# Kernel optimization log

Measured on AMD Instinct MI355X. Metric: run time of the kernel, lower is better.

The kernel has to match this reference:

```python
import jax, jax.numpy as jnp
import numpy as np

N = 100_000  # nodes
E = 1_200_000  # edges (avg degree 12)
EPS = 1e-5


def setup_inputs() -> dict:
    key = jax.random.key(0)
    ks = jax.random.split(key, 12)

    def w(k, shape):
        fan_in = shape[0]
        return jax.random.normal(k, shape, dtype=jnp.float32) * (1.0 / np.sqrt(fan_in))

    return {
        "x": jax.random.normal(ks[0], (N, 4), dtype=jnp.float32),
        "edge_index": jax.random.randint(ks[1], (2, E), 0, N, dtype=jnp.int32),
        "W1": w(ks[2], (4, 16)), "b1": jnp.zeros(16, jnp.float32),
        "g1": jnp.ones(16, jnp.float32), "bt1": jnp.zeros(16, jnp.float32),
        "W2": w(ks[3], (16, 32)), "b2": jnp.zeros(32, jnp.float32),
        "g2": jnp.ones(32, jnp.float32), "bt2": jnp.zeros(32, jnp.float32),
        "W3": w(ks[4], (32, 64)), "b3": jnp.zeros(64, jnp.float32),
        "g3": jnp.ones(64, jnp.float32), "bt3": jnp.zeros(64, jnp.float32),
        "Wf1": w(ks[5], (64, 32)), "bf1": jnp.zeros(32, jnp.float32),
        "Wf2": w(ks[6], (32, 16)), "bf2": jnp.zeros(16, jnp.float32),
        "Wf3": w(ks[7], (16, 2)), "bf3": jnp.zeros(2, jnp.float32),
    }


def _gcn_conv(x, W, b, src, dst):
    """PyG GCNConv: self-loops + symmetric deg^-1/2 normalization + scatter-add."""
    n = x.shape[0]
    h = x @ W  # [N, out]
    loop = jnp.arange(n, dtype=src.dtype)
    s = jnp.concatenate([src, loop])  # [E+N]
    d = jnp.concatenate([dst, loop])
    deg = jax.ops.segment_sum(jnp.ones_like(d, dtype=h.dtype), d, num_segments=n)
    dinv = jnp.where(deg > 0, jax.lax.rsqrt(deg), 0.0)
    norm = dinv[s] * dinv[d]  # [E+N]
    out = jax.ops.segment_sum(h[s] * norm[:, None], d, num_segments=n)
    return out + b


def _bn(x, g, bt):
    # BatchNorm1d over node dim (batch statistics, training-mode semantics)
    m = jnp.mean(x, axis=0)
    v = jnp.var(x, axis=0)
    return (x - m) * jax.lax.rsqrt(v + EPS) * g + bt


def reference(x, edge_index, W1, b1, g1, bt1, W2, b2, g2, bt2, W3, b3, g3, bt3,
              Wf1, bf1, Wf2, bf2, Wf3, bf3):
    src, dst = edge_index[0], edge_index[1]
    h = jax.nn.elu(_bn(jax.nn.relu(_gcn_conv(x, W1, b1, src, dst)), g1, bt1))
    h = jax.nn.elu(_bn(jax.nn.relu(_gcn_conv(h, W2, b2, src, dst)), g2, bt2))
    h = jax.nn.elu(_bn(jax.nn.relu(_gcn_conv(h, W3, b3, src, dst)), g3, bt3))
    h = jax.nn.elu(h @ Wf1 + bf1)
    h = jax.nn.elu(h @ Wf2 + bf2)
    h = h @ Wf3 + bf3
    return jax.nn.log_softmax(h, axis=1)
```

## Files before the change

kernel.cpp:

```cpp
#include <hip/hip_runtime.h>
#include <hip/hip_fp16.h>
#include <math.h>

#define BN_EPS 1e-5f

__device__ inline float4 f4add(float4 a, float4 b) {
  return make_float4(a.x + b.x, a.y + b.y, a.z + b.z, a.w + b.w);
}

union H8 {
  float4 f4;
  __half2 h2[4];
};


__global__ void hist_kernel(const int* __restrict__ dst, int* __restrict__ bcount, int e) {
  __shared__ int h[512];
  for (int i = threadIdx.x; i < 512; i += 256) h[i] = 0;
  __syncthreads();
  int stride = gridDim.x * 256;
  for (int i = blockIdx.x * 256 + threadIdx.x; i < e; i += stride)
    atomicAdd(&h[dst[i] >> 8], 1);
  __syncthreads();
  for (int i = threadIdx.x; i < 512; i += 256)
    if (h[i] > 0) atomicAdd(&bcount[i], h[i]);
}

__global__ void scan_buckets(const int* __restrict__ bcount, int* __restrict__ boffset,
                             int* __restrict__ bcursor, int* __restrict__ row_start,
                             int nbuck, int n, int e) {
  __shared__ int sc[512];
  int tid = threadIdx.x;
  int v = (tid < nbuck) ? bcount[tid] : 0;
  sc[tid] = v;
  __syncthreads();
  for (int off = 1; off < 512; off <<= 1) {
    int add = (tid >= off) ? sc[tid - off] : 0;
    __syncthreads();
    sc[tid] += add;
    __syncthreads();
  }
  int excl = sc[tid] - v;
  if (tid <= nbuck) {
    int val = (tid < nbuck) ? excl : e;
    boffset[tid] = val;
    bcursor[tid] = val;
  }
  if (tid == 0) row_start[n] = e;
}

__global__ void partition_kernel(const int* __restrict__ src, const int* __restrict__ dst,
                                 int* __restrict__ bcursor, int2* __restrict__ ebuf, int e) {
  __shared__ int h[512];
  __shared__ int base[512];
  const int BLK_E = 4096;
  int e0 = blockIdx.x * BLK_E;
  int e1 = min(e0 + BLK_E, e);
  for (int i = threadIdx.x; i < 512; i += 256) h[i] = 0;
  __syncthreads();
  for (int i = e0 + threadIdx.x; i < e1; i += 256)
    atomicAdd(&h[dst[i] >> 8], 1);
  __syncthreads();
  for (int i = threadIdx.x; i < 512; i += 256) {
    int c = h[i];
    base[i] = (c > 0) ? atomicAdd(&bcursor[i], c) : 0;
    h[i] = 0;
  }
  __syncthreads();
  for (int i = e0 + threadIdx.x; i < e1; i += 256) {
    int d = dst[i];
    int b = d >> 8;
    int r = atomicAdd(&h[b], 1);
    ebuf[base[b] + r] = make_int2(src[i], d);
  }
}

__global__ void bucket_fill(const int2* __restrict__ ebuf, const int* __restrict__ boffset,
                            int* __restrict__ row_start, float* __restrict__ dinv,
                            int* __restrict__ csr_src, int n) {
  __shared__ int lcnt[256];
  __shared__ int lpre[256];
  int bid = blockIdx.x;
  int nb0 = bid << 8;
  int tid = threadIdx.x;
  int e0 = boffset[bid], e1 = boffset[bid + 1];
  lcnt[tid] = 0;
  __syncthreads();
  for (int j = e0 + tid; j < e1; j += 256)
    atomicAdd(&lcnt[ebuf[j].y - nb0], 1);
  __syncthreads();
  int v = lcnt[tid];
  lpre[tid] = v;
  __syncthreads();
  for (int off = 1; off < 256; off <<= 1) {
    int add = (tid >= off) ? lpre[tid - off] : 0;
    __syncthreads();
    lpre[tid] += add;
    __syncthreads();
  }
  int excl = lpre[tid] - v;
  int node = nb0 + tid;
  if (node < n) {
    row_start[node] = e0 + excl;
    dinv[node] = rsqrtf((float)(v + 1));
  }
  __syncthreads();
  lpre[tid] = excl;
  __syncthreads();
  for (int j = e0 + tid; j < e1; j += 256) {
    int2 ed = ebuf[j];
    int p = atomicAdd(&lpre[ed.y - nb0], 1);
    csr_src[e0 + p] = ed.x;
  }
}

template <int K, int C, bool BN>
__global__ __launch_bounds__(256) void mm_dinv_h(
    const float* __restrict__ X, const float* __restrict__ stats,
    const float* __restrict__ g, const float* __restrict__ bt,
    const float* __restrict__ W, const float* __restrict__ dinv,
    float4* __restrict__ hh, int n) {
  constexpr int GP8 = C / 8;
  __shared__ float w[K * C];
  __shared__ float bsc[K], bsh[K];
  for (int i = threadIdx.x; i < K * C; i += 256) w[i] = W[i];
  if (BN && threadIdx.x < K) {
    int c = threadIdx.x;
    float inv_n = 1.0f / (float)n;
    float m = stats[c] * inv_n;
    float var = fmaxf(stats[K + c] * inv_n - m * m, 0.f);
    float sc = rsqrtf(var + BN_EPS) * g[c];
    bsc[c] = sc;
    bsh[c] = bt[c] - m * sc;
  }
  __syncthreads();

  int idx = blockIdx.x * 256 + threadIdx.x;
  if (idx >= n * GP8) return;
  int nn = idx / GP8;
  int c8 = idx % GP8;

  float acc[8];
#pragma unroll
  for (int t = 0; t < 8; t++) acc[t] = 0.f;

  const float4* row4 = (const float4*)(X + (size_t)nn * K);
#pragma unroll
  for (int k4 = 0; k4 < K / 4; k4++) {
    float4 xv = row4[k4];
#pragma unroll
    for (int j = 0; j < 4; j++) {
      int k = k4 * 4 + j;
      float v = (j == 0) ? xv.x : (j == 1) ? xv.y : (j == 2) ? xv.z : xv.w;
      if (BN) {
        v = v * bsc[k] + bsh[k];
        v = v > 0.f ? v : (expf(v) - 1.f);
      }
      int wb = k * C + c8 * 8;
#pragma unroll
      for (int t = 0; t < 8; t++) acc[t] += v * w[wb + t];
    }
  }
  float dn = dinv[nn];
  H8 o;
#pragma unroll
  for (int q = 0; q < 4; q++)
    o.h2[q] = __float22half2_rn(make_float2(acc[2 * q] * dn, acc[2 * q + 1] * dn));
  hh[idx] = o.f4;
}

template <int C, int LOGGP>
__global__ __launch_bounds__(256) void gather_finalize_h(
    const float4* __restrict__ hh8, const int* __restrict__ row_start,
    const int* __restrict__ csr_src, const float* __restrict__ dinv,
    const float* __restrict__ bias, float4* __restrict__ act4, int n) {
  constexpr int GP = C / 8;
  constexpr int GP4 = C / 4;
  constexpr int NPB = 256 / GP;
  int tid = threadIdx.x;
  int c8 = tid & (GP - 1);
  int local = tid >> LOGGP;
  int n0 = blockIdx.x * NPB + local;
  if (n0 >= n) return;

  float acc[8];
  {
    H8 u;
    u.f4 = hh8[n0 * GP + c8];
#pragma unroll
    for (int q = 0; q < 4; q++) {
      float2 f = __half22float2(u.h2[q]);
      acc[2 * q] = f.x;
      acc[2 * q + 1] = f.y;
    }
  }
  int s = row_start[n0], e0 = row_start[n0 + 1];
  int j = s;
  for (; j + 4 <= e0; j += 4) {
    int i0 = csr_src[j];
    int i1 = csr_src[j + 1];
    int i2 = csr_src[j + 2];
    int i3 = csr_src[j + 3];
    H8 u0, u1, u2, u3;
    u0.f4 = hh8[i0 * GP + c8];
    u1.f4 = hh8[i1 * GP + c8];
    u2.f4 = hh8[i2 * GP + c8];
    u3.f4 = hh8[i3 * GP + c8];
#pragma unroll
    for (int q = 0; q < 4; q++) {
      float2 f0 = __half22float2(u0.h2[q]);
      float2 f1 = __half22float2(u1.h2[q]);
      float2 f2 = __half22float2(u2.h2[q]);
      float2 f3 = __half22float2(u3.h2[q]);
      acc[2 * q] += (f0.x + f1.x) + (f2.x + f3.x);
      acc[2 * q + 1] += (f0.y + f1.y) + (f2.y + f3.y);
    }
  }
  for (; j < e0; j++) {
    H8 u;
    u.f4 = hh8[csr_src[j] * GP + c8];
#pragma unroll
    for (int q = 0; q < 4; q++) {
      float2 f = __half22float2(u.h2[q]);
      acc[2 * q] += f.x;
      acc[2 * q + 1] += f.y;
    }
  }

  float dn = dinv[n0];
  const float4* bias4 = (const float4*)bias;
  float4 blo = bias4[c8 * 2], bhi = bias4[c8 * 2 + 1];
  float4 v0, v1;
  v0.x = fmaxf(dn * acc[0] + blo.x, 0.f);
  v0.y = fmaxf(dn * acc[1] + blo.y, 0.f);
  v0.z = fmaxf(dn * acc[2] + blo.z, 0.f);
  v0.w = fmaxf(dn * acc[3] + blo.w, 0.f);
  v1.x = fmaxf(dn * acc[4] + bhi.x, 0.f);
  v1.y = fmaxf(dn * acc[5] + bhi.y, 0.f);
  v1.z = fmaxf(dn * acc[6] + bhi.z, 0.f);
  v1.w = fmaxf(dn * acc[7] + bhi.w, 0.f);
  act4[n0 * GP4 + c8 * 2] = v0;
  act4[n0 * GP4 + c8 * 2 + 1] = v1;
}

template <int C>
__global__ void stats_kernel(const float4* __restrict__ act4, float* __restrict__ stats, int n) {
  constexpr int GP = C / 4;
  constexpr int NPB = 256 / GP;
  int tid = threadIdx.x;
  int c4 = tid & (GP - 1);
  int local = tid / GP;
  float4 s = make_float4(0.f, 0.f, 0.f, 0.f);
  float4 q = make_float4(0.f, 0.f, 0.f, 0.f);
  for (int n0 = blockIdx.x * NPB + local; n0 < n; n0 += gridDim.x * NPB) {
    float4 v = act4[n0 * GP + c4];
    s = f4add(s, v);
    q.x += v.x * v.x; q.y += v.y * v.y; q.z += v.z * v.z; q.w += v.w * v.w;
  }
  __shared__ float4 redS[256];
  __shared__ float4 redQ[256];
  redS[tid] = s;
  redQ[tid] = q;
  __syncthreads();
#pragma unroll
  for (int off = 128; off >= GP; off >>= 1) {
    if (tid < off) {
      redS[tid] = f4add(redS[tid], redS[tid + off]);
      redQ[tid] = f4add(redQ[tid], redQ[tid + off]);
    }
    __syncthreads();
  }
  if (tid < GP) {
    atomicAdd(&stats[4 * tid + 0], redS[tid].x);
    atomicAdd(&stats[4 * tid + 1], redS[tid].y);
    atomicAdd(&stats[4 * tid + 2], redS[tid].z);
    atomicAdd(&stats[4 * tid + 3], redS[tid].w);
    atomicAdd(&stats[C + 4 * tid + 0], redQ[tid].x);
    atomicAdd(&stats[C + 4 * tid + 1], redQ[tid].y);
    atomicAdd(&stats[C + 4 * tid + 2], redQ[tid].z);
    atomicAdd(&stats[C + 4 * tid + 3], redQ[tid].w);
  }
}


__global__ __launch_bounds__(256) void head_kernel(
    const float* __restrict__ h,
    const float* __restrict__ st3, const float* __restrict__ g3,
    const float* __restrict__ bt3,
    const float* __restrict__ Wf1, const float* __restrict__ bf1,
    const float* __restrict__ Wf2, const float* __restrict__ bf2,
    const float* __restrict__ Wf3, const float* __restrict__ bf3,
    float* __restrict__ out, int n) {
  __shared__ float w1[64 * 32], w2[32 * 16], w3[16 * 2];
  __shared__ float sb1[32], sb2[16], sb3[2];
  __shared__ float bsc[64], bsh[64];
  for (int i = threadIdx.x; i < 64 * 32; i += 256) w1[i] = Wf1[i];
  for (int i = threadIdx.x; i < 32 * 16; i += 256) w2[i] = Wf2[i];
  if (threadIdx.x < 64) {
    int c = threadIdx.x;
    float inv_n = 1.0f / (float)n;
    float m = st3[c] * inv_n;
    float var = fmaxf(st3[64 + c] * inv_n - m * m, 0.f);
    float sc = rsqrtf(var + BN_EPS) * g3[c];
    bsc[c] = sc;
    bsh[c] = bt3[c] - m * sc;
  }
  if (threadIdx.x < 32) {
    w3[threadIdx.x] = Wf3[threadIdx.x];
    sb1[threadIdx.x] = bf1[threadIdx.x];
  }
  if (threadIdx.x < 16) sb2[threadIdx.x] = bf2[threadIdx.x];
  if (threadIdx.x < 2) sb3[threadIdx.x] = bf3[threadIdx.x];
  __syncthreads();

  int n0 = blockIdx.x * 256 + threadIdx.x;
  if (n0 >= n) return;

  const float4* h4 = (const float4*)(h + (size_t)n0 * 64);

  float a1[32];
#pragma unroll
  for (int c = 0; c < 32; c++) a1[c] = sb1[c];

#pragma unroll
  for (int k4 = 0; k4 < 16; k4++) {
    float4 hv = h4[k4];
#pragma unroll
    for (int j = 0; j < 4; j++) {
      int k = k4 * 4 + j;
      float hk = (j == 0) ? hv.x : (j == 1) ? hv.y : (j == 2) ? hv.z : hv.w;
      float v = hk * bsc[k] + bsh[k];
      v = v > 0.f ? v : (expf(v) - 1.f);
#pragma unroll
      for (int c = 0; c < 32; c++) a1[c] += v * w1[k * 32 + c];
    }
  }
#pragma unroll
  for (int c = 0; c < 32; c++) {
    float v = a1[c];
    a1[c] = v > 0.f ? v : (expf(v) - 1.f);
  }

  float a2[16];
#pragma unroll
  for (int c = 0; c < 16; c++) {
    float acc = sb2[c];
#pragma unroll
    for (int k = 0; k < 32; k++) acc += a1[k] * w2[k * 16 + c];
    a2[c] = acc > 0.f ? acc : (expf(acc) - 1.f);
  }
  float z0 = sb3[0], z1 = sb3[1];
#pragma unroll
  for (int k = 0; k < 16; k++) {
    z0 += a2[k] * w3[k * 2 + 0];
    z1 += a2[k] * w3[k * 2 + 1];
  }
  float mx = fmaxf(z0, z1);
  float lse = mx + logf(expf(z0 - mx) + expf(z1 - mx));
  out[n0 * 2 + 0] = z0 - lse;
  out[n0 * 2 + 1] = z1 - lse;
}


extern "C" void kernel_launch(void* const* d_in, const int* in_sizes, int n_in,
                              void* d_out, int out_size, void* d_ws, size_t ws_size,
                              hipStream_t stream) {
  const float* x = (const float*)d_in[0];
  const int* ei = (const int*)d_in[1];
  const float* W1 = (const float*)d_in[2];  const float* b1 = (const float*)d_in[3];
  const float* g1 = (const float*)d_in[4];  const float* bt1 = (const float*)d_in[5];
  const float* W2 = (const float*)d_in[6];  const float* b2 = (const float*)d_in[7];
  const float* g2 = (const float*)d_in[8];  const float* bt2 = (const float*)d_in[9];
  const float* W3 = (const float*)d_in[10]; const float* b3 = (const float*)d_in[11];
  const float* g3 = (const float*)d_in[12]; const float* bt3 = (const float*)d_in[13];
  const float* Wf1 = (const float*)d_in[14]; const float* bf1 = (const float*)d_in[15];
  const float* Wf2 = (const float*)d_in[16]; const float* bf2 = (const float*)d_in[17];
  const float* Wf3 = (const float*)d_in[18]; const float* bf3 = (const float*)d_in[19];
  float* out = (float*)d_out;

  const int N = in_sizes[0] / 4;
  const int E = in_sizes[1] / 2;
  const int* srcp = ei;
  const int* dstp = ei + E;
  const int NBUCK = (N + 255) >> 8;

  char* ws = (char*)d_ws;
  size_t off = 0;
  auto alloc = [&](size_t bytes) {
    off = (off + 255) & ~(size_t)255;
    size_t o = off;
    off += bytes;
    return o;
  };
  float* dinv      = (float*)(ws + alloc((size_t)N * 4));
  int*   row_start = (int*)  (ws + alloc((size_t)(N + 1) * 4));
  int*   bcount    = (int*)  (ws + alloc((size_t)512 * 4));
  int*   boffset   = (int*)  (ws + alloc((size_t)513 * 4));
  int*   bcursor   = (int*)  (ws + alloc((size_t)513 * 4));
  int*   csr_src   = (int*)  (ws + alloc((size_t)E * 4));
  float* stats     = (float*)(ws + alloc((size_t)224 * 4));
  float* bufH      = (float*)(ws + alloc((size_t)N * 64 * 2));
  float* bufAct    = (float*)(ws + alloc((size_t)N * 64 * 4));
  float* st1 = stats;
  float* st2 = stats + 32;
  float* st3 = stats + 96;
  int2*  ebuf = (int2*)bufH;

  hipMemsetAsync(bcount, 0, 512 * 4, stream);
  hipMemsetAsync(stats, 0, 224 * 4, stream);

  int nb256 = (N + 255) / 256;
  const int STATS_BLOCKS = 128;

  hist_kernel<<<512, 256, 0, stream>>>(dstp, bcount, E);
  scan_buckets<<<1, 512, 0, stream>>>(bcount, boffset, bcursor, row_start, NBUCK, N, E);
  partition_kernel<<<(E + 4095) / 4096, 256, 0, stream>>>(srcp, dstp, bcursor, ebuf, E);
  bucket_fill<<<NBUCK, 256, 0, stream>>>(ebuf, boffset, row_start, dinv, csr_src, N);

  mm_dinv_h<4, 16, false><<<(N * 2 + 255) / 256, 256, 0, stream>>>(
      x, nullptr, nullptr, nullptr, W1, dinv, (float4*)bufH, N);
  gather_finalize_h<16, 1><<<(N + 127) / 128, 256, 0, stream>>>(
      (const float4*)bufH, row_start, csr_src, dinv, b1, (float4*)bufAct, N);
  stats_kernel<16><<<STATS_BLOCKS, 256, 0, stream>>>((const float4*)bufAct, st1, N);

  mm_dinv_h<16, 32, true><<<(N * 4 + 255) / 256, 256, 0, stream>>>(
      bufAct, st1, g1, bt1, W2, dinv, (float4*)bufH, N);
  gather_finalize_h<32, 2><<<(N + 63) / 64, 256, 0, stream>>>(
      (const float4*)bufH, row_start, csr_src, dinv, b2, (float4*)bufAct, N);
  stats_kernel<32><<<STATS_BLOCKS, 256, 0, stream>>>((const float4*)bufAct, st2, N);

  mm_dinv_h<32, 64, true><<<(N * 8 + 255) / 256, 256, 0, stream>>>(
      bufAct, st2, g2, bt2, W3, dinv, (float4*)bufH, N);
  gather_finalize_h<64, 3><<<(N + 31) / 32, 256, 0, stream>>>(
      (const float4*)bufH, row_start, csr_src, dinv, b3, (float4*)bufAct, N);
  stats_kernel<64><<<STATS_BLOCKS, 256, 0, stream>>>((const float4*)bufAct, st3, N);

  head_kernel<<<nb256, 256, 0, stream>>>(bufAct, st3, g3, bt3,
                                         Wf1, bf1, Wf2, bf2, Wf3, bf3, out, N);
}
```

Before: 243.8 us.

## Fuse BN statistics into gather kernel, pack edge buffer, unroll gathers by eight

The BatchNorm sum and sum-of-squares are now computed inside the gather/finalize kernel as per-block partials, followed by a small reduce kernel. This replaces the separate stats pass that re-read the full activation buffer. The edge partition buffer packs src and the low eight bits of dst into a single int, halving that scratch traffic. Other changes: the gather loop is unrolled by eight, and the two memsets are merged into one. In exchange it adds shared-memory reductions and extra syncs per gather block, and the packing assumes src fits in 24 bits.

Measured after the change: 215.4 us. -11.6%, faster.

```diff
diff --git a/kernel.cpp b/kernel.cpp
--- a/kernel.cpp
+++ b/kernel.cpp
@@ -50,7 +50,7 @@
 }
 
 __global__ void partition_kernel(const int* __restrict__ src, const int* __restrict__ dst,
-                                 int* __restrict__ bcursor, int2* __restrict__ ebuf, int e) {
+                                 int* __restrict__ bcursor, int* __restrict__ ebuf, int e) {
   __shared__ int h[512];
   __shared__ int base[512];
   const int BLK_E = 4096;
@@ -71,11 +71,11 @@
     int d = dst[i];
     int b = d >> 8;
     int r = atomicAdd(&h[b], 1);
-    ebuf[base[b] + r] = make_int2(src[i], d);
-  }
-}
-
-__global__ void bucket_fill(const int2* __restrict__ ebuf, const int* __restrict__ boffset,
+    ebuf[base[b] + r] = (src[i] << 8) | (d & 255);
+  }
+}
+
+__global__ void bucket_fill(const int* __restrict__ ebuf, const int* __restrict__ boffset,
                             int* __restrict__ row_start, float* __restrict__ dinv,
                             int* __restrict__ csr_src, int n) {
   __shared__ int lcnt[256];
@@ -87,7 +87,7 @@
   lcnt[tid] = 0;
   __syncthreads();
   for (int j = e0 + tid; j < e1; j += 256)
-    atomicAdd(&lcnt[ebuf[j].y - nb0], 1);
+    atomicAdd(&lcnt[ebuf[j] & 255], 1);
   __syncthreads();
   int v = lcnt[tid];
   lpre[tid] = v;
@@ -108,9 +108,9 @@
   lpre[tid] = excl;
   __syncthreads();
   for (int j = e0 + tid; j < e1; j += 256) {
-    int2 ed = ebuf[j];
-    int p = atomicAdd(&lpre[ed.y - nb0], 1);
-    csr_src[e0 + p] = ed.x;
+    int ed = ebuf[j];
+    int p = atomicAdd(&lpre[ed & 255], 1);
+    csr_src[e0 + p] = ed >> 8;
   }
 }
 
@@ -173,7 +173,8 @@
 __global__ __launch_bounds__(256) void gather_finalize_h(
     const float4* __restrict__ hh8, const int* __restrict__ row_start,
     const int* __restrict__ csr_src, const float* __restrict__ dinv,
-    const float* __restrict__ bias, float4* __restrict__ act4, int n) {
+    const float* __restrict__ bias, float4* __restrict__ act4,
+    float* __restrict__ partials, int n) {
   constexpr int GP = C / 8;
   constexpr int GP4 = C / 4;
   constexpr int NPB = 256 / GP;
@@ -181,105 +182,127 @@
   int c8 = tid & (GP - 1);
   int local = tid >> LOGGP;
   int n0 = blockIdx.x * NPB + local;
-  if (n0 >= n) return;
-
-  float acc[8];
-  {
-    H8 u;
-    u.f4 = hh8[n0 * GP + c8];
-#pragma unroll
-    for (int q = 0; q < 4; q++) {
-      float2 f = __half22float2(u.h2[q]);
-      acc[2 * q] = f.x;
-      acc[2 * q + 1] = f.y;
-    }
-  }
-  int s = row_start[n0], e0 = row_start[n0 + 1];
-  int j = s;
-  for (; j + 4 <= e0; j += 4) {
-    int i0 = csr_src[j];
-    int i1 = csr_src[j + 1];
-    int i2 = csr_src[j + 2];
-    int i3 = csr_src[j + 3];
-    H8 u0, u1, u2, u3;
-    u0.f4 = hh8[i0 * GP + c8];
-    u1.f4 = hh8[i1 * GP + c8];
-    u2.f4 = hh8[i2 * GP + c8];
-    u3.f4 = hh8[i3 * GP + c8];
-#pragma unroll
-    for (int q = 0; q < 4; q++) {
-      float2 f0 = __half22float2(u0.h2[q]);
-      float2 f1 = __half22float2(u1.h2[q]);
-      float2 f2 = __half22float2(u2.h2[q]);
-      float2 f3 = __half22float2(u3.h2[q]);
-      acc[2 * q] += (f0.x + f1.x) + (f2.x + f3.x);
-      acc[2 * q + 1] += (f0.y + f1.y) + (f2.y + f3.y);
-    }
-  }
-  for (; j < e0; j++) {
-    H8 u;
-    u.f4 = hh8[csr_src[j] * GP + c8];
-#pragma unroll
-    for (int q = 0; q < 4; q++) {
-      float2 f = __half22float2(u.h2[q]);
-      acc[2 * q] += f.x;
-      acc[2 * q + 1] += f.y;
-    }
-  }
-
-  float dn = dinv[n0];
-  const float4* bias4 = (const float4*)bias;
-  float4 blo = bias4[c8 * 2], bhi = bias4[c8 * 2 + 1];
-  float4 v0, v1;
-  v0.x = fmaxf(dn * acc[0] + blo.x, 0.f);
-  v0.y = fmaxf(dn * acc[1] + blo.y, 0.f);
-  v0.z = fmaxf(dn * acc[2] + blo.z, 0.f);
-  v0.w = fmaxf(dn * acc[3] + blo.w, 0.f);
-  v1.x = fmaxf(dn * acc[4] + bhi.x, 0.f);
-  v1.y = fmaxf(dn * acc[5] + bhi.y, 0.f);
-  v1.z = fmaxf(dn * acc[6] + bhi.z, 0.f);
-  v1.w = fmaxf(dn * acc[7] + bhi.w, 0.f);
-  act4[n0 * GP4 + c8 * 2] = v0;
-  act4[n0 * GP4 + c8 * 2 + 1] = v1;
-}
-
-template <int C>
-__global__ void stats_kernel(const float4* __restrict__ act4, float* __restrict__ stats, int n) {
-  constexpr int GP = C / 4;
-  constexpr int NPB = 256 / GP;
+  bool valid = (n0 < n);
+
+  float vo[8];
+#pragma unroll
+  for (int t = 0; t < 8; t++) vo[t] = 0.f;
+
+  if (valid) {
+    float acc[8];
+    {
+      H8 u;
+      u.f4 = hh8[n0 * GP + c8];
+#pragma unroll
+      for (int q = 0; q < 4; q++) {
+        float2 f = __half22float2(u.h2[q]);
+        acc[2 * q] = f.x;
+        acc[2 * q + 1] = f.y;
+      }
+    }
+    int s = row_start[n0], e0 = row_start[n0 + 1];
+    int j = s;
+    for (; j + 8 <= e0; j += 8) {
+      H8 u[8];
+#pragma unroll
+      for (int m = 0; m < 8; m++) u[m].f4 = hh8[csr_src[j + m] * GP + c8];
+#pragma unroll
+      for (int m = 0; m < 8; m++)
+#pragma unroll
+        for (int q = 0; q < 4; q++) {
+          float2 f = __half22float2(u[m].h2[q]);
+          acc[2 * q] += f.x;
+          acc[2 * q + 1] += f.y;
+        }
+    }
+    for (; j + 4 <= e0; j += 4) {
+      H8 u[4];
+#pragma unroll
+      for (int m = 0; m < 4; m++) u[m].f4 = hh8[csr_src[j + m] * GP + c8];
+#pragma unroll
+      for (int m = 0; m < 4; m++)
+#pragma unroll
+        for (int q = 0; q < 4; q++) {
+          float2 f = __half22float2(u[m].h2[q]);
+          acc[2 * q] += f.x;
+          acc[2 * q + 1] += f.y;
+        }
+    }
+    for (; j < e0; j++) {
+      H8 u;
+      u.f4 = hh8[csr_src[j] * GP + c8];
+#pragma unroll
+      for (int q = 0; q < 4; q++) {
+        float2 f = __half22float2(u.h2[q]);
+        acc[2 * q] += f.x;
+        acc[2 * q + 1] += f.y;
+      }
+    }
+
+    float dn = dinv[n0];
+    const float4* bias4 = (const float4*)bias;
+    float4 blo = bias4[c8 * 2], bhi = bias4[c8 * 2 + 1];
+    vo[0] = fmaxf(dn * acc[0] + blo.x, 0.f);
+    vo[1] = fmaxf(dn * acc[1] + blo.y, 0.f);
+    vo[2] = fmaxf(dn * acc[2] + blo.z, 0.f);
+    vo[3] = fmaxf(dn * acc[3] + blo.w, 0.f);
+    vo[4] = fmaxf(dn * acc[4] + bhi.x, 0.f);
+    vo[5] = fmaxf(dn * acc[5] + bhi.y, 0.f);
+    vo[6] = fmaxf(dn * acc[6] + bhi.z, 0.f);
+    vo[7] = fmaxf(dn * acc[7] + bhi.w, 0.f);
+    float4 v0 = make_float4(vo[0], vo[1], vo[2], vo[3]);
+    float4 v1 = make_float4(vo[4], vo[5], vo[6], vo[7]);
+    act4[n0 * GP4 + c8 * 2] = v0;
+    act4[n0 * GP4 + c8 * 2 + 1] = v1;
+  }
+
+  __shared__ float redS[8 * 256];
+  __shared__ float redQ[8 * 256];
+#pragma unroll
+  for (int t = 0; t < 8; t++) {
+    redS[t * 256 + tid] = vo[t];
+    redQ[t * 256 + tid] = vo[t] * vo[t];
+  }
+#pragma unroll
+  for (int off = NPB / 2; off >= 1; off >>= 1) {
+    __syncthreads();
+    if (local < off) {
+#pragma unroll
+      for (int t = 0; t < 8; t++) {
+        redS[t * 256 + tid] += redS[t * 256 + tid + off * GP];
+        redQ[t * 256 + tid] += redQ[t * 256 + tid + off * GP];
+      }
+    }
+  }
+  __syncthreads();
+  if (local == 0) {
+#pragma unroll
+    for (int t = 0; t < 8; t++) {
+      partials[(size_t)blockIdx.x * 2 * C + c8 * 8 + t] = redS[t * 256 + tid];
+      partials[(size_t)blockIdx.x * 2 * C + C + c8 * 8 + t] = redQ[t * 256 + tid];
+    }
+  }
+}
+
+template <int C2>
+__global__ void reduce_partials(const float* __restrict__ partials,
+                                float* __restrict__ stats, int rows) {
+  constexpr int NSLOT = 256 / C2;
   int tid = threadIdx.x;
-  int c4 = tid & (GP - 1);
-  int local = tid / GP;
-  float4 s = make_float4(0.f, 0.f, 0.f, 0.f);
-  float4 q = make_float4(0.f, 0.f, 0.f, 0.f);
-  for (int n0 = blockIdx.x * NPB + local; n0 < n; n0 += gridDim.x * NPB) {
-    float4 v = act4[n0 * GP + c4];
-    s = f4add(s, v);
-    q.x += v.x * v.x; q.y += v.y * v.y; q.z += v.z * v.z; q.w += v.w * v.w;
-  }
-  __shared__ float4 redS[256];
-  __shared__ float4 redQ[256];
-  redS[tid] = s;
-  redQ[tid] = q;
-  __syncthreads();
-#pragma unroll
-  for (int off = 128; off >= GP; off >>= 1) {
-    if (tid < off) {
-      redS[tid] = f4add(redS[tid], redS[tid + off]);
-      redQ[tid] = f4add(redQ[tid], redQ[tid + off]);
-    }
-    __syncthreads();
-  }
-  if (tid < GP) {
-    atomicAdd(&stats[4 * tid + 0], redS[tid].x);
-    atomicAdd(&stats[4 * tid + 1], redS[tid].y);
-    atomicAdd(&stats[4 * tid + 2], redS[tid].z);
-    atomicAdd(&stats[4 * tid + 3], redS[tid].w);
-    atomicAdd(&stats[C + 4 * tid + 0], redQ[tid].x);
-    atomicAdd(&stats[C + 4 * tid + 1], redQ[tid].y);
-    atomicAdd(&stats[C + 4 * tid + 2], redQ[tid].z);
-    atomicAdd(&stats[C + 4 * tid + 3], redQ[tid].w);
-  }
+  int ch = tid & (C2 - 1);
+  int slot = tid / C2;
+  float acc = 0.f;
+  for (int r = blockIdx.x * NSLOT + slot; r < rows; r += gridDim.x * NSLOT)
+    acc += partials[(size_t)r * C2 + ch];
+  __shared__ float red[256];
+  red[tid] = acc;
+  __syncthreads();
+#pragma unroll
+  for (int off = 128; off >= C2; off >>= 1) {
+    if (tid < off) red[tid] += red[tid + off];
+    __syncthreads();
+  }
+  if (tid < C2) atomicAdd(&stats[tid], red[tid]);
 }
 
 
@@ -394,46 +417,48 @@
   };
   float* dinv      = (float*)(ws + alloc((size_t)N * 4));
   int*   row_start = (int*)  (ws + alloc((size_t)(N + 1) * 4));
-  int*   bcount    = (int*)  (ws + alloc((size_t)512 * 4));
+  int*   bcount    = (int*)  (ws + alloc((size_t)(512 + 224) * 4));
+  float* stats     = (float*)(bcount + 512);
   int*   boffset   = (int*)  (ws + alloc((size_t)513 * 4));
   int*   bcursor   = (int*)  (ws + alloc((size_t)513 * 4));
   int*   csr_src   = (int*)  (ws + alloc((size_t)E * 4));
-  float* stats     = (float*)(ws + alloc((size_t)224 * 4));
+  float* partials  = (float*)(ws + alloc((size_t)3200 * 128 * 4));
   float* bufH      = (float*)(ws + alloc((size_t)N * 64 * 2));
   float* bufAct    = (float*)(ws + alloc((size_t)N * 64 * 4));
   float* st1 = stats;
   float* st2 = stats + 32;
   float* st3 = stats + 96;
-  int2*  ebuf = (int2*)bufH;
-
-  hipMemsetAsync(bcount, 0, 512 * 4, stream);
-  hipMemsetAsync(stats, 0, 224 * 4, stream);
+  int*   ebuf = (int*)bufH;
+
+  hipMemsetAsync(bcount, 0, (512 + 224) * 4, stream);
 
   int nb256 = (N + 255) / 256;
-  const int STATS_BLOCKS = 128;
 
   hist_kernel<<<512, 256, 0, stream>>>(dstp, bcount, E);
   scan_buckets<<<1, 512, 0, stream>>>(bcount, boffset, bcursor, row_start, NBUCK, N, E);
   partition_kernel<<<(E + 4095) / 4096, 256, 0, stream>>>(srcp, dstp, bcursor, ebuf, E);
   bucket_fill<<<NBUCK, 256, 0, stream>>>(ebuf, boffset, row_start, dinv, csr_src, N);
 
+  int g1n = (N + 127) / 128;
   mm_dinv_h<4, 16, false><<<(N * 2 + 255) / 256, 256, 0, stream>>>(
       x, nullptr, nullptr, nullptr, W1, dinv, (float4*)bufH, N);
-  gather_finalize_h<16, 1><<<(N + 127) / 128, 256, 0, stream>>>(
-      (const float4*)bufH, row_start, csr_src, dinv, b1, (float4*)bufAct, N);
-  stats_kernel<16><<<STATS_BLOCKS, 256, 0, stream>>>((const float4*)bufAct, st1, N);
-
+  gather_finalize_h<16, 1><<<g1n, 256, 0, stream>>>(
+      (const float4*)bufH, row_start, csr_src, dinv, b1, (float4*)bufAct, partials, N);
+  reduce_partials<32><<<64, 256, 0, stream>>>(partials, st1, g1n);
+
+  int g2n = (N + 63) / 64;
   mm_dinv_h<16, 32, true><<<(N * 4 + 255) / 256, 256, 0, stream>>>(
       bufAct, st1, g1, bt1, W2, dinv, (float4*)bufH, N);
-  gather_finalize_h<32, 2><<<(N + 63) / 64, 256, 0, stream>>>(
-      (const float4*)bufH, row_start, csr_src, dinv, b2, (float4*)bufAct, N);
-  stats_kernel<32><<<STATS_BLOCKS, 256, 0, stream>>>((const float4*)bufAct, st2, N);
-
+  gather_finalize_h<32, 2><<<g2n, 256, 0, stream>>>(
+      (const float4*)bufH, row_start, csr_src, dinv, b2, (float4*)bufAct, partials, N);
+  reduce_partials<64><<<64, 256, 0, stream>>>(partials, st2, g2n);
+
+  int g3n = (N + 31) / 32;
   mm_dinv_h<32, 64, true><<<(N * 8 + 255) / 256, 256, 0, stream>>>(
       bufAct, st2, g2, bt2, W3, dinv, (float4*)bufH, N);
-  gather_finalize_h<64, 3><<<(N + 31) / 32, 256, 0, stream>>>(
-      (const float4*)bufH, row_start, csr_src, dinv, b3, (float4*)bufAct, N);
-  stats_kernel<64><<<STATS_BLOCKS, 256, 0, stream>>>((const float4*)bufAct, st3, N);
+  gather_finalize_h<64, 3><<<g3n, 256, 0, stream>>>(
+      (const float4*)bufH, row_start, csr_src, dinv, b3, (float4*)bufAct, partials, N);
+  reduce_partials<128><<<64, 256, 0, stream>>>(partials, st3, g3n);
 
   head_kernel<<<nb256, 256, 0, stream>>>(bufAct, st3, g3, bt3,
                                          Wf1, bf1, Wf2, bf2, Wf3, bf3, out, N);
```
